# Performance work log

Hardware: AMD Instinct MI355X
Metric: run time of the kernel (lower is better)

## Reference

```python
import jax, jax.numpy as jnp
import numpy as np

COST_CLASS, COST_BBOX, COST_MASK = 1.0, 5.0, 2.0
EPS = 1e-6


def setup_inputs() -> dict:
    key = jax.random.key(0)
    k = jax.random.split(key, 8)
    B, Q, M, C1, H, W = 8, 300, 100, 81, 128, 128
    pred_logits = jax.random.normal(k[0], (B, Q, C1), jnp.float32)
    # boxes as valid xyxy in [0,1]: lo in [0,.5], size in [0,.5]
    plo = jax.random.uniform(k[1], (B, Q, 2)) * 0.5
    psz = jax.random.uniform(k[2], (B, Q, 2)) * 0.5
    pred_boxes = jnp.concatenate([plo, plo + psz], axis=-1)
    pred_masks = jax.random.normal(k[3], (B, Q, H, W), jnp.float32)
    gt_labels = jax.random.randint(k[4], (B, M), 0, C1, dtype=jnp.int32)
    glo = jax.random.uniform(k[5], (B, M, 2)) * 0.5
    gsz = jax.random.uniform(k[6], (B, M, 2)) * 0.5
    gt_boxes = jnp.concatenate([glo, glo + gsz], axis=-1)
    gt_masks = (jax.random.uniform(k[7], (B, M, H, W)) > 0.5).astype(jnp.float32)
    valid = jnp.ones((B, M), jnp.bool_)
    return dict(pred_logits=pred_logits, pred_boxes=pred_boxes, pred_masks=pred_masks,
                gt_labels=gt_labels, gt_boxes=gt_boxes, gt_masks=gt_masks, valid=valid)


def _giou(b1, b2):
    # b1 [Q,4], b2 [M,4] (xyxy) -> [Q,M] generalized IoU
    lt = jnp.maximum(b1[:, None, :2], b2[None, :, :2])
    rb = jnp.minimum(b1[:, None, 2:], b2[None, :, 2:])
    wh = jnp.clip(rb - lt, 0.0)
    inter = wh[..., 0] * wh[..., 1]
    a1 = (b1[:, 2] - b1[:, 0]) * (b1[:, 3] - b1[:, 1])
    a2 = (b2[:, 2] - b2[:, 0]) * (b2[:, 3] - b2[:, 1])
    union = a1[:, None] + a2[None, :] - inter
    iou = inter / (union + EPS)
    ltm = jnp.minimum(b1[:, None, :2], b2[None, :, :2])
    rbm = jnp.maximum(b1[:, None, 2:], b2[None, :, 2:])
    whm = jnp.clip(rbm - ltm, 0.0)
    am = whm[..., 0] * whm[..., 1]
    return iou - (am - union) / (am + EPS)


@jax.jit
def _cost_matrix(pred_logits, pred_boxes, pred_masks, gt_labels, gt_boxes, gt_masks):
    B, Q = pred_logits.shape[:2]
    M = gt_labels.shape[1]
    probs = jax.nn.softmax(pred_logits, axis=-1)                      # [B,Q,C+1]
    idx = jnp.broadcast_to(gt_labels[:, None, :].astype(jnp.int32), (B, Q, M))
    cost_class = -jnp.take_along_axis(probs, idx, axis=2)             # [B,Q,M]
    # L1 cdist
    cost_bbox = jnp.abs(pred_boxes[:, :, None, :] - gt_boxes[:, None, :, :]).sum(-1)
    cost_giou = -jax.vmap(_giou)(pred_boxes, gt_boxes)                # [B,Q,M]
    # dice cost
    pm = jax.nn.sigmoid(pred_masks).reshape(B, Q, -1)                 # [B,Q,HW]
    gm = gt_masks.reshape(B, M, -1).astype(pm.dtype)                  # [B,M,HW]
    num = 2.0 * jnp.einsum('bqc,bmc->bqm', pm, gm)
    den = pm.sum(-1)[:, :, None] + gm.sum(-1)[:, None, :]
    cost_mask = 1.0 - num / (den + EPS)
    # NOTE: faithful to source quirk -- giou term is folded into cost_bbox
    # and therefore weighted by COST_BBOX.
    return (COST_CLASS * cost_class + COST_BBOX * (cost_bbox + cost_giou)
            + COST_MASK * cost_mask)


def _hungarian(cost):
    # Jonker-Volgenant style shortest-augmenting-path assignment (e-maxx).
    # cost: np [n,m] with n <= m. Returns p[m]: row assigned to each col (-1 if none).
    n, m = cost.shape
    u = np.zeros(n)
    v = np.zeros(m)
    p = np.full(m, -1, np.int64)
    for i in range(n):
        minv = np.full(m, np.inf)
        way = np.full(m, -1, np.int64)
        used = np.zeros(m, bool)
        cur_row, j0 = i, -1
        while True:
            cur = cost[cur_row] - u[cur_row] - v
            upd = (~used) & (cur < minv)
            minv[upd] = cur[upd]
            way[upd] = j0
            mv = np.where(used, np.inf, minv)
            j1 = int(np.argmin(mv))
            delta = mv[j1]
            u[i] += delta
            uj = np.nonzero(used)[0]
            if uj.size:
                u[p[uj]] += delta
                v[uj] -= delta
            minv[~used] -= delta
            used[j1] = True
            j0 = j1
            cur_row = p[j1]
            if cur_row == -1:
                break
        j = j0
        while j != -1:
            jp = way[j]
            p[j] = p[jp] if jp != -1 else i
            j = jp
    return p


def reference(pred_logits, pred_boxes, pred_masks, gt_labels, gt_boxes, gt_masks, valid):
    # valid is all-ones (num_gt == max_objects for every sample), so the
    # per-sample variable-size slicing in the torch loop reduces to full M.
    C = _cost_matrix(pred_logits, pred_boxes, pred_masks, gt_labels, gt_boxes, gt_masks)
    Cn = np.asarray(C, dtype=np.float64)
    preds, gts = [], []
    for b in range(Cn.shape[0]):
        # solve on transpose: rows = gt (M=100) <= cols = queries (Q=300)
        p = _hungarian(Cn[b].T)            # p[q] = matched gt index or -1
        q = np.nonzero(p >= 0)[0]          # sorted pred indices (scipy convention)
        preds.append(q)
        gts.append(p[q])
    pred_idx = jnp.asarray(np.stack(preds), dtype=jnp.int32)  # [B, M]
    gt_idx = jnp.asarray(np.stack(gts), dtype=jnp.int32)      # [B, M]
    return C, pred_idx, gt_idx
```

## Files before the change

kernel.cpp:

```cpp
#include <hip/hip_runtime.h>

#define HW 16384
#define NQ 300
#define NM 100
#define NB 8
#define NC 81
#define KCH 1024
#define NKC 16
#define CTP 304

typedef __attribute__((ext_vector_type(8))) short frag8;
typedef __attribute__((ext_vector_type(4))) float float4v;
typedef __attribute__((ext_vector_type(4))) unsigned short ushort4v;

__device__ __forceinline__ unsigned short f2bf(float f) {
  union { float f; unsigned u; } c; c.f = f;
  unsigned r = c.u + 0x7FFFu + ((c.u >> 16) & 1u);
  return (unsigned short)(r >> 16);
}

__global__ __launch_bounds__(256) void prep_kernel(
    const float* __restrict__ pmask, const float* __restrict__ gmask,
    unsigned short* __restrict__ pm, unsigned short* __restrict__ gm,
    float* __restrict__ psum, float* __restrict__ gsum) {
  int row = blockIdx.x;
  int t = threadIdx.x;
  bool isP = row < NB * NQ;
  const float* srcf = isP ? (pmask + (size_t)row * HW)
                          : (gmask + (size_t)(row - NB * NQ) * HW);
  unsigned short* dst = isP ? (pm + (size_t)row * HW)
                            : (gm + (size_t)(row - NB * NQ) * HW);
  const float4v* src = (const float4v*)srcf;
  float s = 0.f;
  for (int i = t; i < HW / 4; i += 256) {
    float4v x = src[i];
    float y0, y1, y2, y3;
    if (isP) {
      y0 = 1.f / (1.f + __expf(-x.x));
      y1 = 1.f / (1.f + __expf(-x.y));
      y2 = 1.f / (1.f + __expf(-x.z));
      y3 = 1.f / (1.f + __expf(-x.w));
    } else { y0 = x.x; y1 = x.y; y2 = x.z; y3 = x.w; }
    s += (y0 + y1) + (y2 + y3);
    ushort4v o = { f2bf(y0), f2bf(y1), f2bf(y2), f2bf(y3) };
    *(ushort4v*)(dst + i * 4) = o;
  }
  for (int off = 32; off > 0; off >>= 1) s += __shfl_xor(s, off, 64);
  __shared__ float red[4];
  int wave = t >> 6, lane = t & 63;
  if (lane == 0) red[wave] = s;
  __syncthreads();
  if (t == 0) {
    float tot = (red[0] + red[1]) + (red[2] + red[3]);
    if (isP) psum[row] = tot; else gsum[row - NB * NQ] = tot;
  }
}

__global__ __launch_bounds__(256) void softmax_kernel(
    const float* __restrict__ logits, float* __restrict__ probs) {
  int wave = threadIdx.x >> 6, lane = threadIdx.x & 63;
  int row = blockIdx.x * 4 + wave;
  const float* in = logits + (size_t)row * NC;
  float x0 = (lane < NC) ? in[lane] : -1e30f;
  float x1 = (lane + 64 < NC) ? in[lane + 64] : -1e30f;
  float mx = fmaxf(x0, x1);
  for (int off = 32; off > 0; off >>= 1) mx = fmaxf(mx, __shfl_xor(mx, off, 64));
  float e0 = (lane < NC) ? __expf(x0 - mx) : 0.f;
  float e1 = (lane + 64 < NC) ? __expf(x1 - mx) : 0.f;
  float s = e0 + e1;
  for (int off = 32; off > 0; off >>= 1) s += __shfl_xor(s, off, 64);
  float inv = 1.f / s;
  if (lane < NC) probs[(size_t)row * NC + lane] = e0 * inv;
  if (lane + 64 < NC) probs[(size_t)row * NC + lane + 64] = e1 * inv;
}

__global__ __launch_bounds__(64) void dot_kernel(
    const unsigned short* __restrict__ pm, const unsigned short* __restrict__ gm,
    float* __restrict__ dotv) {
  int qt = blockIdx.x;
  int b = blockIdx.y >> 4, kc = blockIdx.y & 15;
  int lane = threadIdx.x;
  int q0 = qt * 16;
  int row_a = q0 + (lane & 15);
  int ra = (row_a < NQ) ? row_a : NQ - 1;
  int koff = (lane >> 4) * 8;
  const unsigned short* pA = pm + ((size_t)b * NQ + ra) * HW + kc * KCH + koff;
  const unsigned short* pB0 = gm + (size_t)b * NM * HW + kc * KCH + koff;
  const unsigned short* pB[7];
#pragma unroll
  for (int mt = 0; mt < 7; ++mt) {
    int row_b = mt * 16 + (lane & 15);
    int rb = (row_b < NM) ? row_b : NM - 1;
    pB[mt] = pB0 + (size_t)rb * HW;
  }
  float4v acc[7];
#pragma unroll
  for (int mt = 0; mt < 7; ++mt) acc[mt] = (float4v){0.f, 0.f, 0.f, 0.f};
#pragma unroll 2
  for (int k = 0; k < KCH; k += 32) {
    frag8 a = *(const frag8*)(pA + k);
#pragma unroll
    for (int mt = 0; mt < 7; ++mt) {
      frag8 bb = *(const frag8*)(pB[mt] + k);
      acc[mt] = __builtin_amdgcn_mfma_f32_16x16x32_bf16(a, bb, acc[mt], 0, 0, 0);
    }
  }
#pragma unroll
  for (int mt = 0; mt < 7; ++mt) {
    int cm = mt * 16 + (lane & 15);
    if (cm < NM) {
#pragma unroll
      for (int r = 0; r < 4; ++r) {
        int cq = q0 + (lane >> 4) * 4 + r;
        if (cq < NQ)
          unsafeAtomicAdd(&dotv[((size_t)b * NQ + cq) * NM + cm], acc[mt][r]);
      }
    }
  }
}

__global__ __launch_bounds__(256) void combine_kernel(
    const float* __restrict__ dotv, const float* __restrict__ psum,
    const float* __restrict__ gsum, const float* __restrict__ probs,
    const int* __restrict__ labels, const float* __restrict__ pboxes,
    const float* __restrict__ gboxes, float* __restrict__ outC,
    float* __restrict__ ct) {
  int idx = blockIdx.x * 256 + threadIdx.x;
  if (idx >= NB * NQ * NM) return;
  int b = idx / (NQ * NM);
  int r = idx - b * (NQ * NM);
  int q = r / NM;
  int m = r - q * NM;
  float num = 2.f * dotv[idx];
  float den = psum[b * NQ + q] + gsum[b * NM + m];
  float cmask = 1.f - num / (den + 1e-6f);
  int lab = labels[b * NM + m];
  float cclass = -probs[((size_t)b * NQ + q) * NC + lab];
  const float* pb = pboxes + ((size_t)b * NQ + q) * 4;
  const float* gb = gboxes + ((size_t)b * NM + m) * 4;
  float p0 = pb[0], p1 = pb[1], p2 = pb[2], p3 = pb[3];
  float g0 = gb[0], g1 = gb[1], g2 = gb[2], g3 = gb[3];
  float cbbox = fabsf(p0 - g0) + fabsf(p1 - g1) + fabsf(p2 - g2) + fabsf(p3 - g3);
  float iw = fmaxf(fminf(p2, g2) - fmaxf(p0, g0), 0.f);
  float ih = fmaxf(fminf(p3, g3) - fmaxf(p1, g1), 0.f);
  float inter = iw * ih;
  float a1 = (p2 - p0) * (p3 - p1), a2 = (g2 - g0) * (g3 - g1);
  float uni = a1 + a2 - inter;
  float iou = inter / (uni + 1e-6f);
  float aw = fmaxf(fmaxf(p2, g2) - fminf(p0, g0), 0.f);
  float ah = fmaxf(fmaxf(p3, g3) - fminf(p1, g1), 0.f);
  float am = aw * ah;
  float giou = iou - (am - uni) / (am + 1e-6f);
  float C = cclass + 5.f * (cbbox - giou) + 2.f * cmask;
  outC[idx] = C;
  ct[((size_t)b * NM + m) * CTP + q] = C;
}

extern __shared__ char hsmem[];
__global__ __launch_bounds__(64) void hungarian_kernel(
    const float* __restrict__ ct, float* __restrict__ out) {
  float* cost = (float*)hsmem;
  float* u = (float*)(hsmem + 121600);
  int* p = (int*)(hsmem + 122000);
  int* way = (int*)(hsmem + 123280);
  int* colA = (int*)(hsmem + 124560);
  int* rowUsed = (int*)(hsmem + 124960);
  int* colUsed = (int*)(hsmem + 125360);
  const int b = blockIdx.x;
  const int lane = threadIdx.x;
  const float* a = ct + (size_t)b * NM * CTP;

  for (int i = lane; i < NM * CTP; i += 64) cost[i] = a[i];
  for (int k = lane; k < NM; k += 64) rowUsed[k] = 0;
  float v[5], minv[5];
  int usedR[5];
#pragma unroll
  for (int w = 0; w < 5; ++w) {
    p[lane + 64 * w] = -1;
    colUsed[lane + 64 * w] = 0;
    v[w] = 0.f;
  }
  __syncthreads();

  for (int i = lane; i < NM; i += 64) {
    float mv = __builtin_inff();
    int cj = 0;
    for (int j = 0; j < NQ; ++j) {
      float c = cost[i * CTP + j];
      if (c < mv) { mv = c; cj = j; }
    }
    u[i] = mv;
    colA[i] = cj;
  }
  __syncthreads();
  if (lane == 0) {
    for (int i = 0; i < NM; ++i) {
      int j = colA[i];
      if (!colUsed[j]) { colUsed[j] = 1; p[j] = i; rowUsed[i] = 1; }
    }
  }
  __syncthreads();

  for (int i = 0; i < NM; ++i) {
    if (rowUsed[i]) continue;
#pragma unroll
    for (int w = 0; w < 5; ++w) {
      int j = lane + 64 * w;
      minv[w] = __builtin_inff();
      usedR[w] = (j >= NQ) ? 1 : 0;
      way[j] = -1;
    }
    int cur_row = i;
    int j0 = -1;
    __builtin_amdgcn_wave_barrier();
    while (true) {
      float urow = u[cur_row];
      unsigned long long best = ~0ull;
#pragma unroll
      for (int w = 0; w < 5; ++w) {
        if (!usedR[w]) {
          int j = lane + 64 * w;
          float cur = cost[cur_row * CTP + j] - urow - v[w];
          if (cur < minv[w]) { minv[w] = cur; way[j] = j0; }
          unsigned sb = __float_as_uint(minv[w]);
          sb = (sb >> 31) ? ~sb : (sb | 0x80000000u);
          unsigned long long key = ((unsigned long long)sb << 32) | (unsigned)j;
          if (key < best) best = key;
        }
      }
      for (int off = 32; off > 0; off >>= 1) {
        unsigned long long o = __shfl_xor(best, off, 64);
        if (o < best) best = o;
      }
      int j1 = (int)(best & 0xFFFFFFFFu);
      unsigned sb = (unsigned)(best >> 32);
      float delta = __uint_as_float((sb >> 31) ? (sb ^ 0x80000000u) : ~sb);
      __builtin_amdgcn_wave_barrier();
#pragma unroll
      for (int w = 0; w < 5; ++w) {
        int j = lane + 64 * w;
        if (j < NQ) {
          if (usedR[w]) {
            v[w] -= delta;
            int pj = p[j];
            u[pj] += delta;
          } else {
            minv[w] -= delta;
          }
        }
      }
      if (lane == 0) u[i] += delta;
      __builtin_amdgcn_wave_barrier();
#pragma unroll
      for (int w = 0; w < 5; ++w) {
        if (lane + 64 * w == j1) usedR[w] = 1;
      }
      int nr = p[j1];
      j0 = j1;
      if (nr < 0) break;
      cur_row = nr;
    }
    __builtin_amdgcn_wave_barrier();
    if (lane == 0) {
      int j = j0;
      while (j != -1) {
        int jp = way[j];
        p[j] = (jp != -1) ? p[jp] : i;
        j = jp;
      }
    }
    __syncthreads();
  }
  if (lane == 0) {
    float* po = out + NB * NQ * NM + b * NM;
    float* go = out + NB * NQ * NM + NB * NM + b * NM;
    int cnt = 0;
    for (int j = 0; j < NQ; ++j) {
      int pj = p[j];
      if (pj >= 0) { po[cnt] = (float)j; go[cnt] = (float)pj; ++cnt; }
    }
  }
}

extern "C" void kernel_launch(void* const* d_in, const int* in_sizes, int n_in,
                              void* d_out, int out_size, void* d_ws, size_t ws_size,
                              hipStream_t stream) {
  const float* logits = (const float*)d_in[0];
  const float* pboxes = (const float*)d_in[1];
  const float* pmask  = (const float*)d_in[2];
  const int*   labels = (const int*)d_in[3];
  const float* gboxes = (const float*)d_in[4];
  const float* gmask  = (const float*)d_in[5];
  float* out = (float*)d_out;
  char* ws = (char*)d_ws;

  unsigned short* pm   = (unsigned short*)(ws + 0);
  unsigned short* gmb  = (unsigned short*)(ws + 78643200);
  float* psum  = (float*)(ws + 104857600);
  float* gsum  = (float*)(ws + 104867200);
  float* probs = (float*)(ws + 104870400);
  float* dotv  = (float*)(ws + 105648000);
  float* ct    = (float*)(ws + 106608000);

  hipFuncSetAttribute(reinterpret_cast<const void*>(hungarian_kernel),
                      hipFuncAttributeMaxDynamicSharedMemorySize, 126640);

  hipMemsetAsync(dotv, 0, NB * NQ * NM * sizeof(float), stream);
  hipLaunchKernelGGL(prep_kernel, dim3(NB * NQ + NB * NM), dim3(256), 0, stream,
                     pmask, gmask, pm, gmb, psum, gsum);
  hipLaunchKernelGGL(softmax_kernel, dim3(600), dim3(256), 0, stream, logits, probs);
  hipLaunchKernelGGL(dot_kernel, dim3(19, NB * NKC), dim3(64), 0, stream, pm, gmb, dotv);
  hipLaunchKernelGGL(combine_kernel, dim3((NB * NQ * NM + 255) / 256), dim3(256), 0, stream,
                     dotv, psum, gsum, probs, labels, pboxes, gboxes, out, ct);
  hipLaunchKernelGGL(hungarian_kernel, dim3(NB), dim3(64), 126640, stream, ct, out);
}
```

Before: 516.5 us.

## Replace Hungarian solver with LAPJV-style auction and Dijkstra augmentation

Replaces the per-row Hungarian solver with a Jonker-Volgenant scheme. Two auction-style augmenting-row-reduction passes are followed by a Dijkstra shortest-path augmentation for the rows still free, and the column state is kept in registers and exchanged with shuffles. The cost row pitch is padded to 305 to change the shared-memory bank pattern, and the dot kernel grid is flattened so that batch is the fastest-varying block index. The serial single-wave Hungarian loop is the target. The change risks matching differences on tied costs and relies on the guard counters to bound the loops.

```diff
diff --git a/kernel.cpp b/kernel.cpp
--- a/kernel.cpp
+++ b/kernel.cpp
@@ -7,7 +7,7 @@
 #define NC 81
 #define KCH 1024
 #define NKC 16
-#define CTP 304
+#define CTP 305
 
 typedef __attribute__((ext_vector_type(8))) short frag8;
 typedef __attribute__((ext_vector_type(4))) float float4v;
@@ -18,6 +18,31 @@
   unsigned r = c.u + 0x7FFFu + ((c.u >> 16) & 1u);
   return (unsigned short)(r >> 16);
 }
+
+__device__ __forceinline__ unsigned long long packkey(float f, int j) {
+  unsigned u = __float_as_uint(f);
+  u = (u >> 31) ? ~u : (u | 0x80000000u);
+  return ((unsigned long long)u << 32) | (unsigned)j;
+}
+__device__ __forceinline__ float unpackkey(unsigned long long k) {
+  unsigned sb = (unsigned)(k >> 32);
+  return __uint_as_float((sb >> 31) ? (sb ^ 0x80000000u) : ~sb);
+}
+
+#define GET5I(arr, j, res) { int _w = (j) >> 6; int _v = arr[0]; \
+  if (_w == 1) _v = arr[1]; else if (_w == 2) _v = arr[2]; \
+  else if (_w == 3) _v = arr[3]; else if (_w == 4) _v = arr[4]; \
+  res = __shfl(_v, (j) & 63, 64); }
+#define GET5F(arr, j, res) { int _w = (j) >> 6; float _v = arr[0]; \
+  if (_w == 1) _v = arr[1]; else if (_w == 2) _v = arr[2]; \
+  else if (_w == 3) _v = arr[3]; else if (_w == 4) _v = arr[4]; \
+  res = __shfl(_v, (j) & 63, 64); }
+#define SET5I(arr, w1, val) { switch (w1) { case 0: arr[0] = val; break; \
+  case 1: arr[1] = val; break; case 2: arr[2] = val; break; \
+  case 3: arr[3] = val; break; default: arr[4] = val; break; } }
+#define SUB5F(arr, w1, val) { switch (w1) { case 0: arr[0] -= val; break; \
+  case 1: arr[1] -= val; break; case 2: arr[2] -= val; break; \
+  case 3: arr[3] -= val; break; default: arr[4] -= val; break; } }
 
 __global__ __launch_bounds__(256) void prep_kernel(
     const float* __restrict__ pmask, const float* __restrict__ gmask,
@@ -77,8 +102,11 @@
 __global__ __launch_bounds__(64) void dot_kernel(
     const unsigned short* __restrict__ pm, const unsigned short* __restrict__ gm,
     float* __restrict__ dotv) {
-  int qt = blockIdx.x;
-  int b = blockIdx.y >> 4, kc = blockIdx.y & 15;
+  int blk = blockIdx.x;
+  int b = blk & 7;
+  int t = blk >> 3;
+  int qt = t % 19;
+  int kc = t / 19;
   int lane = threadIdx.x;
   int q0 = qt * 16;
   int row_a = q0 + (lane & 15);
@@ -160,125 +188,156 @@
 __global__ __launch_bounds__(64) void hungarian_kernel(
     const float* __restrict__ ct, float* __restrict__ out) {
   float* cost = (float*)hsmem;
-  float* u = (float*)(hsmem + 121600);
-  int* p = (int*)(hsmem + 122000);
-  int* way = (int*)(hsmem + 123280);
-  int* colA = (int*)(hsmem + 124560);
-  int* rowUsed = (int*)(hsmem + 124960);
-  int* colUsed = (int*)(hsmem + 125360);
+  int* colsolL = (int*)(hsmem + 122000);
+  int* rowsolL = (int*)(hsmem + 123280);
+  int* predL   = (int*)(hsmem + 123680);
+  int* freeL   = (int*)(hsmem + 124960);
   const int b = blockIdx.x;
   const int lane = threadIdx.x;
   const float* a = ct + (size_t)b * NM * CTP;
 
   for (int i = lane; i < NM * CTP; i += 64) cost[i] = a[i];
-  for (int k = lane; k < NM; k += 64) rowUsed[k] = 0;
-  float v[5], minv[5];
-  int usedR[5];
-#pragma unroll
-  for (int w = 0; w < 5; ++w) {
-    p[lane + 64 * w] = -1;
-    colUsed[lane + 64 * w] = 0;
-    v[w] = 0.f;
-  }
+  for (int i = lane; i < NM; i += 64) { rowsolL[i] = -1; freeL[i] = i; }
+  float vv[5]; int cs[5];
+#pragma unroll
+  for (int w = 0; w < 5; ++w) { vv[w] = 0.f; cs[w] = -1; colsolL[lane + 64 * w] = -1; }
   __syncthreads();
 
-  for (int i = lane; i < NM; i += 64) {
-    float mv = __builtin_inff();
-    int cj = 0;
-    for (int j = 0; j < NQ; ++j) {
-      float c = cost[i * CTP + j];
-      if (c < mv) { mv = c; cj = j; }
-    }
-    u[i] = mv;
-    colA[i] = cj;
-  }
-  __syncthreads();
-  if (lane == 0) {
-    for (int i = 0; i < NM; ++i) {
-      int j = colA[i];
-      if (!colUsed[j]) { colUsed[j] = 1; p[j] = i; rowUsed[i] = 1; }
-    }
-  }
-  __syncthreads();
-
-  for (int i = 0; i < NM; ++i) {
-    if (rowUsed[i]) continue;
-#pragma unroll
-    for (int w = 0; w < 5; ++w) {
-      int j = lane + 64 * w;
-      minv[w] = __builtin_inff();
-      usedR[w] = (j >= NQ) ? 1 : 0;
-      way[j] = -1;
-    }
-    int cur_row = i;
-    int j0 = -1;
-    __builtin_amdgcn_wave_barrier();
-    while (true) {
-      float urow = u[cur_row];
-      unsigned long long best = ~0ull;
-#pragma unroll
-      for (int w = 0; w < 5; ++w) {
-        if (!usedR[w]) {
-          int j = lane + 64 * w;
-          float cur = cost[cur_row * CTP + j] - urow - v[w];
-          if (cur < minv[w]) { minv[w] = cur; way[j] = j0; }
-          unsigned sb = __float_as_uint(minv[w]);
-          sb = (sb >> 31) ? ~sb : (sb | 0x80000000u);
-          unsigned long long key = ((unsigned long long)sb << 32) | (unsigned)j;
-          if (key < best) best = key;
-        }
-      }
-      for (int off = 32; off > 0; off >>= 1) {
-        unsigned long long o = __shfl_xor(best, off, 64);
-        if (o < best) best = o;
-      }
-      int j1 = (int)(best & 0xFFFFFFFFu);
-      unsigned sb = (unsigned)(best >> 32);
-      float delta = __uint_as_float((sb >> 31) ? (sb ^ 0x80000000u) : ~sb);
-      __builtin_amdgcn_wave_barrier();
+  int nfree = NM;
+  for (int pass = 0; pass < 2; ++pass) {
+    int prv = nfree, k = 0, nf2 = 0, guard = 0;
+    while (k < prv && guard < 1500) {
+      ++guard;
+      int i = freeL[k]; ++k;
+      unsigned long long k1 = ~0ull, k2 = ~0ull;
 #pragma unroll
       for (int w = 0; w < 5; ++w) {
         int j = lane + 64 * w;
         if (j < NQ) {
-          if (usedR[w]) {
-            v[w] -= delta;
-            int pj = p[j];
-            u[pj] += delta;
-          } else {
-            minv[w] -= delta;
-          }
+          unsigned long long key = packkey(cost[i * CTP + j] - vv[w], j);
+          if (key < k1) { k2 = k1; k1 = key; }
+          else if (key < k2) k2 = key;
         }
       }
-      if (lane == 0) u[i] += delta;
+#pragma unroll
+      for (int off = 32; off > 0; off >>= 1) {
+        unsigned long long o1 = __shfl_xor(k1, off, 64);
+        unsigned long long o2 = __shfl_xor(k2, off, 64);
+        unsigned long long n1 = (k1 < o1) ? k1 : o1;
+        unsigned long long mx = (k1 < o1) ? o1 : k1;
+        unsigned long long n2 = (k2 < o2) ? k2 : o2;
+        if (mx < n2) n2 = mx;
+        k1 = n1; k2 = n2;
+      }
+      int j1 = (int)(unsigned)k1;
+      int j2 = (int)(unsigned)k2;
+      float umin = unpackkey(k1), usub = unpackkey(k2);
+      int i0; GET5I(cs, j1, i0);
+      bool strict = (umin < usub);
+      if (strict) {
+        if (lane == (j1 & 63)) { int w1 = j1 >> 6; float dlt = usub - umin; SUB5F(vv, w1, dlt); }
+      } else if (i0 >= 0) {
+        j1 = j2;
+        GET5I(cs, j2, i0);
+      }
+      if (lane == (j1 & 63)) { int w1 = j1 >> 6; SET5I(cs, w1, i); }
+      if (lane == 0) { colsolL[j1] = i; rowsolL[i] = j1; }
+      if (i0 >= 0) {
+        if (lane == 0) rowsolL[i0] = -1;
+        if (strict) { --k; if (lane == 0) freeL[k] = i0; }
+        else { if (lane == 0) freeL[nf2] = i0; ++nf2; }
+      }
       __builtin_amdgcn_wave_barrier();
+    }
+    while (k < prv) {
+      int lr = freeL[k]; ++k;
+      if (lane == 0) freeL[nf2] = lr;
+      ++nf2;
+      __builtin_amdgcn_wave_barrier();
+    }
+    nfree = nf2;
+  }
+
+  for (int f = 0; f < nfree; ++f) {
+    int irow = freeL[f];
+    float d[5]; int pr[5], sc[5];
+#pragma unroll
+    for (int w = 0; w < 5; ++w) {
+      int j = lane + 64 * w;
+      if (j < NQ) { d[w] = cost[irow * CTP + j] - vv[w]; sc[w] = 0; }
+      else { d[w] = 1e30f; sc[w] = 1; }
+      pr[w] = irow;
+    }
+    float mind = 0.f; int endj = -1;
+    for (int pop = 0; pop < 310; ++pop) {
+      unsigned long long k1 = ~0ull;
+#pragma unroll
+      for (int w = 0; w < 5; ++w)
+        if (!sc[w]) { unsigned long long key = packkey(d[w], lane + 64 * w); if (key < k1) k1 = key; }
+#pragma unroll
+      for (int off = 32; off > 0; off >>= 1) {
+        unsigned long long o = __shfl_xor(k1, off, 64);
+        if (o < k1) k1 = o;
+      }
+      int j1 = (int)(unsigned)k1;
+      mind = unpackkey(k1);
+      int i0; GET5I(cs, j1, i0);
+      if (i0 < 0) { endj = j1; break; }
+      if (lane == (j1 & 63)) { int w1 = j1 >> 6; SET5I(sc, w1, 1); }
+      float rv[5];
 #pragma unroll
       for (int w = 0; w < 5; ++w) {
-        if (lane + 64 * w == j1) usedR[w] = 1;
-      }
-      int nr = p[j1];
-      j0 = j1;
-      if (nr < 0) break;
-      cur_row = nr;
-    }
+        int j = lane + 64 * w;
+        rv[w] = (j < NQ) ? cost[i0 * CTP + j] : 0.f;
+      }
+      float cij1; GET5F(rv, j1, cij1);
+      float vj1;  GET5F(vv, j1, vj1);
+      float h = cij1 - vj1 - mind;
+#pragma unroll
+      for (int w = 0; w < 5; ++w) {
+        int j = lane + 64 * w;
+        if (j < NQ && !sc[w]) {
+          float nd = rv[w] - vv[w] - h;
+          if (nd < d[w]) { d[w] = nd; pr[w] = i0; }
+        }
+      }
+    }
+#pragma unroll
+    for (int w = 0; w < 5; ++w) {
+      int j = lane + 64 * w;
+      if (j < NQ && sc[w]) vv[w] += d[w] - mind;
+    }
+#pragma unroll
+    for (int w = 0; w < 5; ++w) predL[lane + 64 * w] = pr[w];
     __builtin_amdgcn_wave_barrier();
-    if (lane == 0) {
-      int j = j0;
-      while (j != -1) {
-        int jp = way[j];
-        p[j] = (jp != -1) ? p[jp] : i;
-        j = jp;
-      }
-    }
-    __syncthreads();
-  }
-  if (lane == 0) {
-    float* po = out + NB * NQ * NM + b * NM;
-    float* go = out + NB * NQ * NM + NB * NM + b * NM;
-    int cnt = 0;
-    for (int j = 0; j < NQ; ++j) {
-      int pj = p[j];
-      if (pj >= 0) { po[cnt] = (float)j; go[cnt] = (float)pj; ++cnt; }
-    }
+    if (lane == 0 && endj >= 0) {
+      int j = endj;
+      while (true) {
+        int ii = predL[j];
+        colsolL[j] = ii;
+        int jn = rowsolL[ii];
+        rowsolL[ii] = j;
+        if (ii == irow) break;
+        j = jn;
+      }
+    }
+    __builtin_amdgcn_wave_barrier();
+#pragma unroll
+    for (int w = 0; w < 5; ++w) cs[w] = colsolL[lane + 64 * w];
+    __builtin_amdgcn_wave_barrier();
+  }
+
+  float* po = out + NB * NQ * NM + b * NM;
+  float* go = out + NB * NQ * NM + NB * NM + b * NM;
+  int base = 0;
+#pragma unroll
+  for (int w = 0; w < 5; ++w) {
+    int j = lane + 64 * w;
+    bool valid = (j < NQ) && (cs[w] >= 0);
+    unsigned long long mask = __ballot(valid);
+    int pos = base + __popcll(mask & ((1ull << lane) - 1ull));
+    if (valid) { po[pos] = (float)j; go[pos] = (float)cs[w]; }
+    base += __popcll(mask);
   }
 }
 
@@ -303,14 +362,14 @@
   float* ct    = (float*)(ws + 106608000);
 
   hipFuncSetAttribute(reinterpret_cast<const void*>(hungarian_kernel),
-                      hipFuncAttributeMaxDynamicSharedMemorySize, 126640);
+                      hipFuncAttributeMaxDynamicSharedMemorySize, 125472);
 
   hipMemsetAsync(dotv, 0, NB * NQ * NM * sizeof(float), stream);
   hipLaunchKernelGGL(prep_kernel, dim3(NB * NQ + NB * NM), dim3(256), 0, stream,
                      pmask, gmask, pm, gmb, psum, gsum);
   hipLaunchKernelGGL(softmax_kernel, dim3(600), dim3(256), 0, stream, logits, probs);
-  hipLaunchKernelGGL(dot_kernel, dim3(19, NB * NKC), dim3(64), 0, stream, pm, gmb, dotv);
+  hipLaunchKernelGGL(dot_kernel, dim3(8 * 19 * NKC), dim3(64), 0, stream, pm, gmb, dotv);
   hipLaunchKernelGGL(combine_kernel, dim3((NB * NQ * NM + 255) / 256), dim3(256), 0, stream,
                      dotv, psum, gsum, probs, labels, pboxes, gboxes, out, ct);
-  hipLaunchKernelGGL(hungarian_kernel, dim3(NB), dim3(64), 126640, stream, ct, out);
-}
+  hipLaunchKernelGGL(hungarian_kernel, dim3(NB), dim3(64), 125472, stream, ct, out);
+}
```

New measurement: 557.1 us. 1.08x slower.
